# Performance work log

Measured on AMD Instinct MI355X. Metric: run time of the kernel, lower is better.

Reference implementation:

```python
import jax, jax.numpy as jnp
import numpy as np

N = 50000
E = 500000
H = 128


def setup_inputs() -> dict:
    key = jax.random.key(0)
    ks = jax.random.split(key, 7)
    x = jax.random.normal(ks[0], (N, 4, H), dtype=jnp.float32)
    edge_index = jax.random.randint(ks[1], (2, E), 0, N, dtype=jnp.int64)
    s = 1.0 / np.sqrt(H)
    W_s_rel = jax.random.normal(ks[2], (H, H), dtype=jnp.float32) * s
    W_s_root = jax.random.normal(ks[3], (H, H), dtype=jnp.float32) * s
    b_s_root = jax.random.normal(ks[4], (H,), dtype=jnp.float32) * s
    W_v_rel = jax.random.normal(ks[5], (H, H), dtype=jnp.float32) * s
    W_v_root = jax.random.normal(ks[6], (H, H), dtype=jnp.float32) * s
    return {"x": x, "edge_index": edge_index, "W_s_rel": W_s_rel,
            "W_s_root": W_s_root, "b_s_root": b_s_root,
            "W_v_rel": W_v_rel, "W_v_root": W_v_root}


def reference(x, edge_index, W_s_rel, W_s_root, b_s_root, W_v_rel, W_v_root):
    # x: (N, 4, H); channel 0 is scalar, channels 1:4 are a 3-vector per feature
    scalar = x[:, 0, :]          # (N, H)
    vector = x[:, 1:, :]         # (N, 3, H)
    row, col = edge_index[0], edge_index[1]
    n = scalar.shape[0]

    # Per-edge messages: gather source (col) features, project with rel weights
    scalar_msg = scalar[col] @ W_s_rel.T                     # (E, H)
    vector_msg = jnp.einsum('evh,oh->evo', vector[col], W_v_rel)  # (E, 3, H)

    # Scatter-add into destination (row) nodes
    scalar_agg = jax.ops.segment_sum(scalar_msg, row, num_segments=n)
    vector_agg = jax.ops.segment_sum(vector_msg, row, num_segments=n)

    scalar_out = scalar @ W_s_root.T + b_s_root + scalar_agg          # (N, H)
    vector_out = jnp.einsum('nvh,oh->nvo', vector, W_v_root) + vector_agg  # (N, 3, H)

    return jnp.concatenate([scalar_out[:, None, :], vector_out], axis=1)  # (N, 4, H)
```

## Files before the change

### kernel.cpp

```cpp
#include <hip/hip_runtime.h>


typedef short bfrag __attribute__((ext_vector_type(8)));
typedef float cfrag __attribute__((ext_vector_type(16)));
typedef float f4v  __attribute__((ext_vector_type(4)));

__device__ __forceinline__ short f2bf(float f) {
    unsigned u = __builtin_bit_cast(unsigned, f);
    u += 0x7fff + ((u >> 16) & 1);
    return (short)(u >> 16);
}
__device__ __forceinline__ float bf2f(short s) {
    unsigned u = ((unsigned)(unsigned short)s) << 16;
    return __builtin_bit_cast(float, u);
}
__device__ __forceinline__ bfrag pack8(float4 lo, float4 hi) {
    bfrag r;
    r[0] = f2bf(lo.x); r[1] = f2bf(lo.y); r[2] = f2bf(lo.z); r[3] = f2bf(lo.w);
    r[4] = f2bf(hi.x); r[5] = f2bf(hi.y); r[6] = f2bf(hi.z); r[7] = f2bf(hi.w);
    return r;
}
__device__ __forceinline__ bfrag pack8v(f4v lo, f4v hi) {
    bfrag r;
    r[0] = f2bf(lo[0]); r[1] = f2bf(lo[1]); r[2] = f2bf(lo[2]); r[3] = f2bf(lo[3]);
    r[4] = f2bf(hi[0]); r[5] = f2bf(hi[1]); r[6] = f2bf(hi[2]); r[7] = f2bf(hi[3]);
    return r;
}

__global__ __launch_bounds__(256) void prep0_kernel(
    const float* __restrict__ w0, const float* __restrict__ w1,
    const float* __restrict__ w2, const float* __restrict__ w3,
    short* __restrict__ wbf,
    const int* __restrict__ ei, int* __restrict__ counts, int E)
{
    int b = blockIdx.x;
    if (b < 32) {
        int i = b * 256 + threadIdx.x;
        int j = i * 8;
        int m = j >> 14, off = j & 16383;
        const float* src = (m == 0) ? w0 : (m == 1) ? w1 : (m == 2) ? w2 : w3;
        float4 lo = *(const float4*)(src + off);
        float4 hi = *(const float4*)(src + off + 4);
        *(bfrag*)(wbf + j) = pack8(lo, hi);
    } else {
        int e = (b - 32) * 256 + threadIdx.x;
        if (e < E) atomicAdd(&counts[ei[e]], 1);
    }
}

__global__ __launch_bounds__(1024) void scan_local_kernel(
    const int* __restrict__ counts, int* __restrict__ offsets,
    int* __restrict__ cursor, int* __restrict__ blocksums, int N)
{
    __shared__ int wsum[16];
    const int tid = threadIdx.x, lane = tid & 63, wid = tid >> 6;
    int i = blockIdx.x * 1024 + tid;
    int v = (i < N) ? counts[i] : 0;
    int incl = v;
    #pragma unroll
    for (int off = 1; off < 64; off <<= 1) {
        int t = __shfl_up(incl, off, 64);
        if (lane >= off) incl += t;
    }
    if (lane == 63) wsum[wid] = incl;
    __syncthreads();
    if (wid == 0) {
        int ws = (lane < 16) ? wsum[lane] : 0;
        int wincl = ws;
        #pragma unroll
        for (int off = 1; off < 16; off <<= 1) {
            int t = __shfl_up(wincl, off, 64);
            if (lane >= off) wincl += t;
        }
        if (lane < 16) wsum[lane] = wincl - ws;
    }
    __syncthreads();
    int excl = incl - v + wsum[wid];
    if (i < N) { offsets[i] = excl; cursor[i] = excl; }
    if (tid == 1023) blocksums[blockIdx.x] = excl + v;
}

__global__ __launch_bounds__(256) void mega_kernel(
    const int* __restrict__ ei, int* __restrict__ cursor,
    int* __restrict__ bins, int E,
    int* __restrict__ offsets, const int* __restrict__ blocksums,
    int nb, int N,
    const float* __restrict__ x, short* __restrict__ xbf, long long total8,
    int nbin, int nfix)
{
    int b = blockIdx.x;
    if (b < nbin + nfix) {
        __shared__ int pref[64];
        if (threadIdx.x < 64) {
            int lane = threadIdx.x;
            int v = (lane < nb) ? blocksums[lane] : 0;
            int incl = v;
            #pragma unroll
            for (int off = 1; off < 64; off <<= 1) {
                int t = __shfl_up(incl, off, 64);
                if (lane >= off) incl += t;
            }
            pref[lane] = incl - v;
        }
        __syncthreads();
        if (b < nbin) {
            int e = b * 256 + threadIdx.x;
            if (e < E) {
                int row = ei[e], col = ei[E + e];
                int pos = atomicAdd(&cursor[row], 1) + pref[row >> 10];
                bins[pos] = col;
            }
        } else {
            int i = (b - nbin) * 256 + threadIdx.x;
            if (i < N) offsets[i] += pref[i >> 10];
            else if (i == N) offsets[i] = E;
        }
    } else {
        long long i = (long long)(b - nbin - nfix) * 256 + threadIdx.x;
        if (i >= total8) return;
        f4v lo = __builtin_nontemporal_load((const f4v*)(x + i * 8));
        f4v hi = __builtin_nontemporal_load((const f4v*)(x + i * 8 + 4));
        *(bfrag*)(xbf + i * 8) = pack8v(lo, hi);
    }
}

template<int XBF>
__global__ __launch_bounds__(256) void fused_agg_mfma(
    const float* __restrict__ x, const short* __restrict__ xbf,
    const int* __restrict__ offsets, const int* __restrict__ bins,
    float* __restrict__ out, const short* __restrict__ wbf,
    const float* __restrict__ b_s, int Nn)
{
    __shared__ short atile[32 * 512];
    const int tid  = threadIdx.x;
    const int wid  = tid >> 6;
    const int lane = tid & 63;
    const int n0   = blockIdx.x * 32;

    const int cl   = lane >> 4;
    const int slot = lane & 15;
    #pragma unroll 1
    for (int i = 0; i < 8; i++) {
        const int m = wid * 8 + i;
        const int n = n0 + m;
        float acc[8] = {0, 0, 0, 0, 0, 0, 0, 0};
        if (n < Nn) {
            const int beg = offsets[n], end = offsets[n + 1];
            int e = beg;
            if (XBF) {
                for (; e + 8 <= end; e += 8) {
                    int cc[8];
                    #pragma unroll
                    for (int q = 0; q < 8; q++) cc[q] = bins[e + q];
                    bfrag v[8];
                    #pragma unroll
                    for (int q = 0; q < 8; q++)
                        v[q] = *(const bfrag*)(xbf + (size_t)cc[q] * 512 + lane * 8);
                    #pragma unroll
                    for (int j = 0; j < 8; j++)
                        acc[j] += ((bf2f(v[0][j]) + bf2f(v[1][j])) +
                                   (bf2f(v[2][j]) + bf2f(v[3][j]))) +
                                  ((bf2f(v[4][j]) + bf2f(v[5][j])) +
                                   (bf2f(v[6][j]) + bf2f(v[7][j])));
                }
                for (; e + 4 <= end; e += 4) {
                    int c4[4];
                    #pragma unroll
                    for (int q = 0; q < 4; q++) c4[q] = bins[e + q];
                    bfrag v[4];
                    #pragma unroll
                    for (int q = 0; q < 4; q++)
                        v[q] = *(const bfrag*)(xbf + (size_t)c4[q] * 512 + lane * 8);
                    #pragma unroll
                    for (int j = 0; j < 8; j++)
                        acc[j] += (bf2f(v[0][j]) + bf2f(v[1][j])) +
                                  (bf2f(v[2][j]) + bf2f(v[3][j]));
                }
                for (; e < end; e++) {
                    int cc1 = bins[e];
                    bfrag v = *(const bfrag*)(xbf + (size_t)cc1 * 512 + lane * 8);
                    #pragma unroll
                    for (int j = 0; j < 8; j++) acc[j] += bf2f(v[j]);
                }
            } else {
                for (; e < end; e++) {
                    int cc1 = bins[e];
                    float4 l = *(const float4*)(x + (size_t)cc1 * 512 + lane * 8);
                    float4 h = *(const float4*)(x + (size_t)cc1 * 512 + lane * 8 + 4);
                    acc[0] += l.x; acc[1] += l.y; acc[2] += l.z; acc[3] += l.w;
                    acc[4] += h.x; acc[5] += h.y; acc[6] += h.z; acc[7] += h.w;
                }
            }
        }
        const int boff = m * 1024 + cl * 256 + ((slot * 16) ^ ((m & 15) << 4));
        *(bfrag*)((char*)atile + boff) =
            pack8(make_float4(acc[0], acc[1], acc[2], acc[3]),
                  make_float4(acc[4], acc[5], acc[6], acc[7]));
    }

    const int c   = wid;
    const int l31 = lane & 31;
    const int kg  = lane >> 5;
    int mA = n0 + l31; if (mA >= Nn) mA = Nn - 1;
    const size_t arow = ((size_t)mA * 4 + c) * 128;
    bfrag a0[8];
    #pragma unroll
    for (int ks = 0; ks < 8; ks++) {
        const int k0 = ks * 16 + kg * 8;
        if (XBF) {
            a0[ks] = *(const bfrag*)(xbf + arow + k0);
        } else {
            float4 lo = *(const float4*)(x + arow + k0);
            float4 hi = *(const float4*)(x + arow + k0 + 4);
            a0[ks] = pack8(lo, hi);
        }
    }

    __syncthreads();

    const short* wroot = wbf + ((c == 0) ? 0 : 2) * 16384;
    const short* wrel  = wbf + ((c == 0) ? 1 : 3) * 16384;

    cfrag acc4[4];
    #pragma unroll
    for (int t = 0; t < 4; t++)
        #pragma unroll
        for (int r = 0; r < 16; r++) acc4[t][r] = 0.f;

    __builtin_amdgcn_s_setprio(1);
    #pragma unroll
    for (int ks = 0; ks < 8; ks++) {
        const int k0 = ks * 16 + kg * 8;
        const int rboff = l31 * 1024 + c * 256 + ((k0 * 2) ^ ((l31 & 15) << 4));
        bfrag a1 = *(const bfrag*)((const char*)atile + rboff);
        #pragma unroll
        for (int t = 0; t < 4; t++) {
            bfrag b0 = *(const bfrag*)(wroot + (size_t)(t * 32 + l31) * 128 + k0);
            acc4[t] = __builtin_amdgcn_mfma_f32_32x32x16_bf16(a0[ks], b0, acc4[t], 0, 0, 0);
            bfrag b1 = *(const bfrag*)(wrel + (size_t)(t * 32 + l31) * 128 + k0);
            acc4[t] = __builtin_amdgcn_mfma_f32_32x32x16_bf16(a1, b1, acc4[t], 0, 0, 0);
        }
    }
    __builtin_amdgcn_s_setprio(0);

    float bv[4] = {0.f, 0.f, 0.f, 0.f};
    if (c == 0) {
        #pragma unroll
        for (int t = 0; t < 4; t++) bv[t] = b_s[t * 32 + l31];
    }

    #pragma unroll
    for (int t = 0; t < 4; t++) {
        #pragma unroll
        for (int r = 0; r < 16; r++) {
            int row = (r & 3) + 8 * (r >> 2) + 4 * kg;
            int node = n0 + row;
            if (node < Nn)
                __builtin_nontemporal_store(
                    acc4[t][r] + bv[t],
                    out + ((size_t)node * 4 + c) * 128 + t * 32 + l31);
        }
    }
}

extern "C" void kernel_launch(void* const* d_in, const int* in_sizes, int n_in,
                              void* d_out, int out_size, void* d_ws, size_t ws_size,
                              hipStream_t stream) {
    const float* x        = (const float*)d_in[0];
    const int*   ei       = (const int*)d_in[1];
    const float* W_s_rel  = (const float*)d_in[2];
    const float* W_s_root = (const float*)d_in[3];
    const float* b_s_root = (const float*)d_in[4];
    const float* W_v_rel  = (const float*)d_in[5];
    const float* W_v_root = (const float*)d_in[6];
    float* out = (float*)d_out;

    int N = in_sizes[0] / 512;
    int E = in_sizes[1] / 2;

    size_t ints_bytes = ((size_t)(3 * N + 1) + E + 64) * sizeof(int);
    size_t wbf_bytes  = 65536 * sizeof(short);
    size_t xbf_bytes  = (size_t)N * 512 * sizeof(short);
    bool use_bf = (ws_size >= wbf_bytes + xbf_bytes + ints_bytes);

    short* wbf = (short*)d_ws;
    short* xbf = wbf + 65536;
    int* counts = use_bf ? (int*)(xbf + (size_t)N * 512) : (int*)xbf;
    int* offsets   = counts + N;
    int* cursor    = offsets + N + 1;
    int* bins      = cursor + N;
    int* blocksums = bins + E;

    int nb = (N + 1023) / 1024;
    long long total8 = (long long)N * 64;
    int nconv = use_bf ? (int)((total8 + 255) / 256) : 0;
    int nbin  = (E + 255) / 256;
    int nfix  = (N + 1 + 255) / 256;
    int nh    = nbin;

    hipMemsetAsync(counts, 0, (size_t)N * sizeof(int), stream);
    prep0_kernel<<<32 + nh, 256, 0, stream>>>(
        W_s_root, W_s_rel, W_v_root, W_v_rel, wbf, ei, counts, E);
    scan_local_kernel<<<nb, 1024, 0, stream>>>(counts, offsets, cursor, blocksums, N);
    mega_kernel<<<nbin + nfix + nconv, 256, 0, stream>>>(
        ei, cursor, bins, E, offsets, blocksums, nb, N,
        x, xbf, total8, nbin, nfix);

    if (use_bf) {
        fused_agg_mfma<1><<<(N + 31) / 32, 256, 0, stream>>>(
            x, xbf, offsets, bins, out, wbf, b_s_root, N);
    } else {
        fused_agg_mfma<0><<<(N + 31) / 32, 256, 0, stream>>>(
            x, nullptr, offsets, bins, out, wbf, b_s_root, N);
    }
}
```

Before: 377.8 us.

## Fuse all stages into one persistent cooperative kernel with grid syncs

Replaces the memset plus four kernel launches with a single cooperative persistent kernel that zeroes counts, converts the weights and x to bf16, histograms, scans, bins edges and runs the MFMA aggregation tiles, with grid.sync between phases. The aggregation tiles are handed out dynamically through an atomic tile counter. This removes launch gaps and per-kernel tail effects, but adds five grid-wide barriers and caps the grid at the cooperative occupancy limit. If cooperative launch is unavailable it falls back to the original multi-kernel path.

```diff
diff --git a/kernel.cpp b/kernel.cpp
--- a/kernel.cpp
+++ b/kernel.cpp
@@ -1,4 +1,7 @@
 #include <hip/hip_runtime.h>
+#include <hip/hip_cooperative_groups.h>
+
+namespace cg = cooperative_groups;
 
 
 typedef short bfrag __attribute__((ext_vector_type(8)));
@@ -27,116 +30,14 @@
     return r;
 }
 
-__global__ __launch_bounds__(256) void prep0_kernel(
-    const float* __restrict__ w0, const float* __restrict__ w1,
-    const float* __restrict__ w2, const float* __restrict__ w3,
-    short* __restrict__ wbf,
-    const int* __restrict__ ei, int* __restrict__ counts, int E)
-{
-    int b = blockIdx.x;
-    if (b < 32) {
-        int i = b * 256 + threadIdx.x;
-        int j = i * 8;
-        int m = j >> 14, off = j & 16383;
-        const float* src = (m == 0) ? w0 : (m == 1) ? w1 : (m == 2) ? w2 : w3;
-        float4 lo = *(const float4*)(src + off);
-        float4 hi = *(const float4*)(src + off + 4);
-        *(bfrag*)(wbf + j) = pack8(lo, hi);
-    } else {
-        int e = (b - 32) * 256 + threadIdx.x;
-        if (e < E) atomicAdd(&counts[ei[e]], 1);
-    }
-}
-
-__global__ __launch_bounds__(1024) void scan_local_kernel(
-    const int* __restrict__ counts, int* __restrict__ offsets,
-    int* __restrict__ cursor, int* __restrict__ blocksums, int N)
-{
-    __shared__ int wsum[16];
-    const int tid = threadIdx.x, lane = tid & 63, wid = tid >> 6;
-    int i = blockIdx.x * 1024 + tid;
-    int v = (i < N) ? counts[i] : 0;
-    int incl = v;
-    #pragma unroll
-    for (int off = 1; off < 64; off <<= 1) {
-        int t = __shfl_up(incl, off, 64);
-        if (lane >= off) incl += t;
-    }
-    if (lane == 63) wsum[wid] = incl;
-    __syncthreads();
-    if (wid == 0) {
-        int ws = (lane < 16) ? wsum[lane] : 0;
-        int wincl = ws;
-        #pragma unroll
-        for (int off = 1; off < 16; off <<= 1) {
-            int t = __shfl_up(wincl, off, 64);
-            if (lane >= off) wincl += t;
-        }
-        if (lane < 16) wsum[lane] = wincl - ws;
-    }
-    __syncthreads();
-    int excl = incl - v + wsum[wid];
-    if (i < N) { offsets[i] = excl; cursor[i] = excl; }
-    if (tid == 1023) blocksums[blockIdx.x] = excl + v;
-}
-
-__global__ __launch_bounds__(256) void mega_kernel(
-    const int* __restrict__ ei, int* __restrict__ cursor,
-    int* __restrict__ bins, int E,
-    int* __restrict__ offsets, const int* __restrict__ blocksums,
-    int nb, int N,
-    const float* __restrict__ x, short* __restrict__ xbf, long long total8,
-    int nbin, int nfix)
-{
-    int b = blockIdx.x;
-    if (b < nbin + nfix) {
-        __shared__ int pref[64];
-        if (threadIdx.x < 64) {
-            int lane = threadIdx.x;
-            int v = (lane < nb) ? blocksums[lane] : 0;
-            int incl = v;
-            #pragma unroll
-            for (int off = 1; off < 64; off <<= 1) {
-                int t = __shfl_up(incl, off, 64);
-                if (lane >= off) incl += t;
-            }
-            pref[lane] = incl - v;
-        }
-        __syncthreads();
-        if (b < nbin) {
-            int e = b * 256 + threadIdx.x;
-            if (e < E) {
-                int row = ei[e], col = ei[E + e];
-                int pos = atomicAdd(&cursor[row], 1) + pref[row >> 10];
-                bins[pos] = col;
-            }
-        } else {
-            int i = (b - nbin) * 256 + threadIdx.x;
-            if (i < N) offsets[i] += pref[i >> 10];
-            else if (i == N) offsets[i] = E;
-        }
-    } else {
-        long long i = (long long)(b - nbin - nfix) * 256 + threadIdx.x;
-        if (i >= total8) return;
-        f4v lo = __builtin_nontemporal_load((const f4v*)(x + i * 8));
-        f4v hi = __builtin_nontemporal_load((const f4v*)(x + i * 8 + 4));
-        *(bfrag*)(xbf + i * 8) = pack8v(lo, hi);
-    }
-}
-
 template<int XBF>
-__global__ __launch_bounds__(256) void fused_agg_mfma(
+__device__ __forceinline__ void fused_tile_body(
     const float* __restrict__ x, const short* __restrict__ xbf,
     const int* __restrict__ offsets, const int* __restrict__ bins,
     float* __restrict__ out, const short* __restrict__ wbf,
-    const float* __restrict__ b_s, int Nn)
-{
-    __shared__ short atile[32 * 512];
-    const int tid  = threadIdx.x;
-    const int wid  = tid >> 6;
-    const int lane = tid & 63;
-    const int n0   = blockIdx.x * 32;
-
+    const float* __restrict__ b_s, int Nn, int n0, short* atile,
+    int tid, int wid, int lane)
+{
     const int cl   = lane >> 4;
     const int slot = lane & 15;
     #pragma unroll 1
@@ -263,6 +164,232 @@
     }
 }
 
+template<int XBF>
+__global__ __launch_bounds__(256) void coop_all(
+    const float* __restrict__ x, short* __restrict__ xbf,
+    const int* __restrict__ ei, int* __restrict__ counts,
+    int* __restrict__ offsets, int* __restrict__ cursor,
+    int* __restrict__ bins, int* __restrict__ blocksums,
+    int* __restrict__ tile_ctr,
+    float* __restrict__ out, short* __restrict__ wbf,
+    const float* __restrict__ w0, const float* __restrict__ w1,
+    const float* __restrict__ w2, const float* __restrict__ w3,
+    const float* __restrict__ b_s, int N, int E, long long total8)
+{
+    __shared__ short atile[32 * 512];
+    __shared__ int tsel;
+    int* ip = (int*)atile;
+    cg::grid_group grid = cg::this_grid();
+    const int tid = threadIdx.x, lane = tid & 63, wid = tid >> 6;
+    const long long gstride = (long long)gridDim.x * 256;
+    const long long gtid = (long long)blockIdx.x * 256 + tid;
+
+    if (gtid == 0) *tile_ctr = 0;
+    for (long long i = gtid; i < N; i += gstride) counts[i] = 0;
+    for (long long i = gtid; i < 8192; i += gstride) {
+        int j = (int)i * 8;
+        int m = j >> 14, off = j & 16383;
+        const float* src = (m == 0) ? w0 : (m == 1) ? w1 : (m == 2) ? w2 : w3;
+        float4 lo = *(const float4*)(src + off);
+        float4 hi = *(const float4*)(src + off + 4);
+        *(bfrag*)(wbf + j) = pack8(lo, hi);
+    }
+    if (XBF) {
+        for (long long i = gtid; i < total8; i += gstride) {
+            f4v lo = __builtin_nontemporal_load((const f4v*)(x + i * 8));
+            f4v hi = __builtin_nontemporal_load((const f4v*)(x + i * 8 + 4));
+            *(bfrag*)(xbf + i * 8) = pack8v(lo, hi);
+        }
+    }
+    grid.sync();
+
+    for (long long e = gtid; e < E; e += gstride)
+        atomicAdd(&counts[ei[e]], 1);
+    grid.sync();
+
+    const int nchunks = (N + 255) >> 8;
+    for (int ch = blockIdx.x; ch < nchunks; ch += gridDim.x) {
+        int i = ch * 256 + tid;
+        int v = (i < N) ? counts[i] : 0;
+        int incl = v;
+        #pragma unroll
+        for (int off = 1; off < 64; off <<= 1) {
+            int t = __shfl_up(incl, off, 64);
+            if (lane >= off) incl += t;
+        }
+        if (lane == 63) ip[wid] = incl;
+        __syncthreads();
+        if (tid == 0) {
+            int s = 0;
+            #pragma unroll
+            for (int k = 0; k < 4; k++) { int t = ip[k]; ip[k] = s; s += t; }
+        }
+        __syncthreads();
+        int excl = incl - v + ip[wid];
+        if (i < N) offsets[i] = excl;
+        if (tid == 255) blocksums[ch] = excl + v;
+        __syncthreads();
+    }
+    grid.sync();
+
+    {
+        int v = (tid < nchunks) ? blocksums[tid] : 0;
+        int incl = v;
+        #pragma unroll
+        for (int off = 1; off < 64; off <<= 1) {
+            int t = __shfl_up(incl, off, 64);
+            if (lane >= off) incl += t;
+        }
+        if (lane == 63) ip[wid] = incl;
+        __syncthreads();
+        if (tid == 0) {
+            int s = 0;
+            #pragma unroll
+            for (int k = 0; k < 4; k++) { int t = ip[k]; ip[k] = s; s += t; }
+        }
+        __syncthreads();
+        int pref = incl - v + ip[wid];
+        __syncthreads();
+        ip[8 + tid] = pref;
+        __syncthreads();
+        for (int ch = blockIdx.x; ch < nchunks; ch += gridDim.x) {
+            int base = ip[8 + ch];
+            int i = ch * 256 + tid;
+            if (i < N) { int vv = offsets[i] + base; offsets[i] = vv; cursor[i] = vv; }
+        }
+        if (blockIdx.x == 0 && tid == 0) offsets[N] = E;
+    }
+    grid.sync();
+
+    for (long long e = gtid; e < E; e += gstride) {
+        int row = ei[e], col = ei[E + e];
+        int pos = atomicAdd(&cursor[row], 1);
+        bins[pos] = col;
+    }
+    grid.sync();
+
+    const int ntiles = (N + 31) >> 5;
+    for (;;) {
+        __syncthreads();
+        if (tid == 0) tsel = atomicAdd(tile_ctr, 1);
+        __syncthreads();
+        int t = tsel;
+        if (t >= ntiles) break;
+        fused_tile_body<XBF>(x, xbf, offsets, bins, out, wbf, b_s,
+                             N, t * 32, atile, tid, wid, lane);
+    }
+}
+
+__global__ __launch_bounds__(256) void prep0_kernel(
+    const float* __restrict__ w0, const float* __restrict__ w1,
+    const float* __restrict__ w2, const float* __restrict__ w3,
+    short* __restrict__ wbf,
+    const int* __restrict__ ei, int* __restrict__ counts, int E)
+{
+    int b = blockIdx.x;
+    if (b < 32) {
+        int i = b * 256 + threadIdx.x;
+        int j = i * 8;
+        int m = j >> 14, off = j & 16383;
+        const float* src = (m == 0) ? w0 : (m == 1) ? w1 : (m == 2) ? w2 : w3;
+        float4 lo = *(const float4*)(src + off);
+        float4 hi = *(const float4*)(src + off + 4);
+        *(bfrag*)(wbf + j) = pack8(lo, hi);
+    } else {
+        int e = (b - 32) * 256 + threadIdx.x;
+        if (e < E) atomicAdd(&counts[ei[e]], 1);
+    }
+}
+
+__global__ __launch_bounds__(1024) void scan_local_kernel(
+    const int* __restrict__ counts, int* __restrict__ offsets,
+    int* __restrict__ cursor, int* __restrict__ blocksums, int N)
+{
+    __shared__ int wsum[16];
+    const int tid = threadIdx.x, lane = tid & 63, wid = tid >> 6;
+    int i = blockIdx.x * 1024 + tid;
+    int v = (i < N) ? counts[i] : 0;
+    int incl = v;
+    #pragma unroll
+    for (int off = 1; off < 64; off <<= 1) {
+        int t = __shfl_up(incl, off, 64);
+        if (lane >= off) incl += t;
+    }
+    if (lane == 63) wsum[wid] = incl;
+    __syncthreads();
+    if (wid == 0) {
+        int ws = (lane < 16) ? wsum[lane] : 0;
+        int wincl = ws;
+        #pragma unroll
+        for (int off = 1; off < 16; off <<= 1) {
+            int t = __shfl_up(wincl, off, 64);
+            if (lane >= off) wincl += t;
+        }
+        if (lane < 16) wsum[lane] = wincl - ws;
+    }
+    __syncthreads();
+    int excl = incl - v + wsum[wid];
+    if (i < N) { offsets[i] = excl; cursor[i] = excl; }
+    if (tid == 1023) blocksums[blockIdx.x] = excl + v;
+}
+
+__global__ __launch_bounds__(256) void mega_kernel(
+    const int* __restrict__ ei, int* __restrict__ cursor,
+    int* __restrict__ bins, int E,
+    int* __restrict__ offsets, const int* __restrict__ blocksums,
+    int nb, int N,
+    const float* __restrict__ x, short* __restrict__ xbf, long long total8,
+    int nbin, int nfix)
+{
+    int b = blockIdx.x;
+    if (b < nbin + nfix) {
+        __shared__ int pref[64];
+        if (threadIdx.x < 64) {
+            int lane = threadIdx.x;
+            int v = (lane < nb) ? blocksums[lane] : 0;
+            int incl = v;
+            #pragma unroll
+            for (int off = 1; off < 64; off <<= 1) {
+                int t = __shfl_up(incl, off, 64);
+                if (lane >= off) incl += t;
+            }
+            pref[lane] = incl - v;
+        }
+        __syncthreads();
+        if (b < nbin) {
+            int e = b * 256 + threadIdx.x;
+            if (e < E) {
+                int row = ei[e], col = ei[E + e];
+                int pos = atomicAdd(&cursor[row], 1) + pref[row >> 10];
+                bins[pos] = col;
+            }
+        } else {
+            int i = (b - nbin) * 256 + threadIdx.x;
+            if (i < N) offsets[i] += pref[i >> 10];
+            else if (i == N) offsets[i] = E;
+        }
+    } else {
+        long long i = (long long)(b - nbin - nfix) * 256 + threadIdx.x;
+        if (i >= total8) return;
+        f4v lo = __builtin_nontemporal_load((const f4v*)(x + i * 8));
+        f4v hi = __builtin_nontemporal_load((const f4v*)(x + i * 8 + 4));
+        *(bfrag*)(xbf + i * 8) = pack8v(lo, hi);
+    }
+}
+
+template<int XBF>
+__global__ __launch_bounds__(256) void fused_agg_mfma(
+    const float* __restrict__ x, const short* __restrict__ xbf,
+    const int* __restrict__ offsets, const int* __restrict__ bins,
+    float* __restrict__ out, const short* __restrict__ wbf,
+    const float* __restrict__ b_s, int Nn)
+{
+    __shared__ short atile[32 * 512];
+    fused_tile_body<XBF>(x, xbf, offsets, bins, out, wbf, b_s,
+                         Nn, blockIdx.x * 32, atile,
+                         threadIdx.x, threadIdx.x >> 6, threadIdx.x & 63);
+}
+
 extern "C" void kernel_launch(void* const* d_in, const int* in_sizes, int n_in,
                               void* d_out, int out_size, void* d_ws, size_t ws_size,
                               hipStream_t stream) {
@@ -278,28 +405,61 @@
     int N = in_sizes[0] / 512;
     int E = in_sizes[1] / 2;
 
-    size_t ints_bytes = ((size_t)(3 * N + 1) + E + 64) * sizeof(int);
+    size_t ints_bytes = ((size_t)(3 * N + 1) + E + 257) * sizeof(int);
     size_t wbf_bytes  = 65536 * sizeof(short);
     size_t xbf_bytes  = (size_t)N * 512 * sizeof(short);
     bool use_bf = (ws_size >= wbf_bytes + xbf_bytes + ints_bytes);
 
     short* wbf = (short*)d_ws;
-    short* xbf = wbf + 65536;
-    int* counts = use_bf ? (int*)(xbf + (size_t)N * 512) : (int*)xbf;
+    short* xbf = use_bf ? (wbf + 65536) : nullptr;
+    int* counts = use_bf ? (int*)(wbf + 65536 + (size_t)N * 512)
+                         : (int*)(wbf + 65536);
     int* offsets   = counts + N;
     int* cursor    = offsets + N + 1;
     int* bins      = cursor + N;
     int* blocksums = bins + E;
+    int* tile_ctr  = blocksums + 256;
+
+    long long total8 = use_bf ? (long long)N * 64 : 0;
+
+    static int coop_grid = -2;
+    if (coop_grid == -2) {
+        int dev = 0;
+        hipGetDevice(&dev);
+        int coop = 0;
+        hipDeviceGetAttribute(&coop, hipDeviceAttributeCooperativeLaunch, dev);
+        if (coop) {
+            hipDeviceProp_t prop{};
+            hipGetDeviceProperties(&prop, dev);
+            int nbpc = 0;
+            hipOccupancyMaxActiveBlocksPerMultiprocessor(&nbpc, coop_all<1>, 256, 0);
+            coop_grid = (nbpc > 0 && prop.multiProcessorCount > 0)
+                      ? nbpc * prop.multiProcessorCount : -1;
+        } else {
+            coop_grid = -1;
+        }
+    }
+
+    if (coop_grid > 0 && N <= 65536) {
+        void* kf = use_bf ? (void*)&coop_all<1> : (void*)&coop_all<0>;
+        void* args[] = {
+            (void*)&x, (void*)&xbf, (void*)&ei, (void*)&counts,
+            (void*)&offsets, (void*)&cursor, (void*)&bins, (void*)&blocksums,
+            (void*)&tile_ctr, (void*)&out, (void*)&wbf,
+            (void*)&W_s_root, (void*)&W_s_rel, (void*)&W_v_root, (void*)&W_v_rel,
+            (void*)&b_s_root, (void*)&N, (void*)&E, (void*)&total8
+        };
+        hipLaunchCooperativeKernel(kf, dim3(coop_grid), dim3(256), args, 0, stream);
+        return;
+    }
 
     int nb = (N + 1023) / 1024;
-    long long total8 = (long long)N * 64;
     int nconv = use_bf ? (int)((total8 + 255) / 256) : 0;
     int nbin  = (E + 255) / 256;
     int nfix  = (N + 1 + 255) / 256;
-    int nh    = nbin;
 
     hipMemsetAsync(counts, 0, (size_t)N * sizeof(int), stream);
-    prep0_kernel<<<32 + nh, 256, 0, stream>>>(
+    prep0_kernel<<<32 + nbin, 256, 0, stream>>>(
         W_s_root, W_s_rel, W_v_root, W_v_rel, wbf, ei, counts, E);
     scan_local_kernel<<<nb, 1024, 0, stream>>>(counts, offsets, cursor, blocksums, N);
     mega_kernel<<<nbin + nfix + nconv, 256, 0, stream>>>(
```

Result: no change. 378.2 us (+0.1%).
